# Performance work log

Hardware: AMD Instinct MI355X
Metric: run time of the kernel (lower is better)

Reference implementation:

```python
import jax, jax.numpy as jnp
import numpy as np

B, C, D = 2, 2048, 1024   # batch, seq_len, hidden_size
I = 2048                  # intermediate_size (GLU hidden)
E, K = 8, 2               # n_experts, top_k
CF = 1.25                 # capacity factor


def setup_inputs() -> dict:
    key = jax.random.key(0)
    k1, k2, k3, k4 = jax.random.split(key, 4)
    scale = 0.02
    return {
        "hidden_states": jax.random.normal(k1, (B, C, D), jnp.float32),
        "Wg": jax.random.normal(k2, (E, D), jnp.float32) * scale,      # router gate weight [E, d]
        "W1": jax.random.normal(k3, (E, D, 2 * I), jnp.float32) * scale,  # expert in-proj
        "W2": jax.random.normal(k4, (E, I, D), jnp.float32) * scale,      # expert out-proj
    }


def reference(hidden_states, Wg, W1, W2):
    Bx, Cx, d = hidden_states.shape
    N = Bx * Cx
    cap = int(N * K * CF / E)  # exp_capacity (static)
    x = hidden_states.reshape(N, d)

    # --- router (eval mode: no noise) ---
    logits = x @ Wg.T                          # [N, E]
    top_v, top_i = jax.lax.top_k(logits, K)    # [N, K]
    gates = jax.nn.softmax(top_v, axis=-1)     # [N, K]

    # --- greedy capacity-limited assignment (token-major, then k), vectorized ---
    flat_e = top_i.reshape(N * K)              # expert id per (token, k) slot, in loop order
    gates_f = gates.reshape(N * K)
    tok = jnp.repeat(jnp.arange(N), K)         # token id per slot
    onehot = jax.nn.one_hot(flat_e, E, dtype=jnp.int32)
    pos = jnp.cumsum(onehot, axis=0) - 1       # running count per expert
    pos_f = jnp.take_along_axis(pos, flat_e[:, None], axis=1)[:, 0]
    keep = pos_f < cap                         # slots beyond capacity are dropped
    pos_safe = jnp.where(keep, pos_f, cap)     # out-of-range -> dropped by mode='drop'

    # --- dispatch: exp_batches[e, pos] = x[token] ---
    exp_batches = jnp.zeros((E, cap, d), x.dtype).at[flat_e, pos_safe].set(x[tok], mode='drop')

    # --- per-expert GLU MLP (batched over experts) ---
    h = jnp.einsum('ecd,edf->ecf', exp_batches, W1)       # [E, cap, 2I]
    inp, gate = jnp.split(h, 2, axis=-1)
    h = jax.nn.gelu(inp, approximate=False) * gate        # exact gelu, matches torch
    exp_out = jnp.einsum('eci,eid->ecd', h, W2)           # [E, cap, d]

    # --- combine: equals exp_mask.view(N,-1) @ exp_out.view(-1,d) ---
    gathered = exp_out[flat_e, jnp.minimum(pos_safe, cap - 1)]  # [N*K, d]
    contrib = jnp.where(keep, gates_f, 0.0)[:, None] * gathered
    out = jax.ops.segment_sum(contrib, tok, num_segments=N)    # [N, d]
    return out.reshape(Bx, Cx, d)
```

## Files before the change

kernel.cpp:

```cpp
#include <hip/hip_runtime.h>
#include <hip/hip_bf16.h>
#include <math.h>

#define N_TOK 4096
#define DIM   1024
#define NEXP  8
#define IDIM  2048
#define TWOI  4096
#define CAP   1280

using short8  = __attribute__((ext_vector_type(8))) short;
using floatx4 = __attribute__((ext_vector_type(4))) float;

__device__ __forceinline__ unsigned short f2b(float f) {
  __hip_bfloat16 h = __float2bfloat16(f);
  return *reinterpret_cast<unsigned short*>(&h);
}

__device__ __forceinline__ void async16(const unsigned short* g, unsigned short* l) {
  __builtin_amdgcn_global_load_lds(
      (const __attribute__((address_space(1))) unsigned int*)g,
      (__attribute__((address_space(3))) unsigned int*)l,
      16, 0, 0);
}


__global__ __launch_bounds__(256) void conv_x_kernel(const float* __restrict__ x,
                                                     unsigned short* __restrict__ xb) {
  int i = (blockIdx.x * 256 + threadIdx.x) * 4;
  float4 v = *reinterpret_cast<const float4*>(x + i);
  ushort4 o;
  o.x = f2b(v.x); o.y = f2b(v.y); o.z = f2b(v.z); o.w = f2b(v.w);
  *reinterpret_cast<ushort4*>(xb + i) = o;
}

__global__ __launch_bounds__(256) void transpose_kernel(const float* __restrict__ src,
                                                        unsigned short* __restrict__ dst,
                                                        int R, int C) {
  __shared__ float tile[32][33];
  int e  = blockIdx.z;
  int c0 = blockIdx.x * 32, r0 = blockIdx.y * 32;
  int tx = threadIdx.x & 31, ty = threadIdx.x >> 5;
  const float* s = src + (size_t)e * R * C;
  unsigned short* d = dst + (size_t)e * R * C;
#pragma unroll
  for (int i = 0; i < 4; i++) {
    int r = ty + i * 8;
    tile[r][tx] = s[(size_t)(r0 + r) * C + c0 + tx];
  }
  __syncthreads();
#pragma unroll
  for (int i = 0; i < 4; i++) {
    int c = ty + i * 8;
    d[(size_t)(c0 + c) * R + r0 + tx] = f2b(tile[tx][c]);
  }
}

__global__ __launch_bounds__(256) void router_kernel(const float* __restrict__ x,
                                                     const float* __restrict__ Wg,
                                                     int* __restrict__ top_i,
                                                     float* __restrict__ gates) {
  __shared__ float wg[NEXP * DIM];
  int tid = threadIdx.x;
  for (int i = tid * 4; i < NEXP * DIM; i += 256 * 4) {
    *reinterpret_cast<float4*>(wg + i) = *reinterpret_cast<const float4*>(Wg + i);
  }
  __syncthreads();
  int wave = tid >> 6, lane = tid & 63;
  int t = blockIdx.x * 4 + wave;
  const float* xr = x + (size_t)t * DIM;
  double acc[NEXP];
#pragma unroll
  for (int e = 0; e < NEXP; e++) acc[e] = 0.0;
  for (int i = lane; i < DIM; i += 64) {
    double xv = (double)xr[i];
#pragma unroll
    for (int e = 0; e < NEXP; e++) acc[e] += xv * (double)wg[e * DIM + i];
  }
#pragma unroll
  for (int e = 0; e < NEXP; e++) {
#pragma unroll
    for (int m = 1; m < 64; m <<= 1) acc[e] += __shfl_xor(acc[e], m, 64);
  }
  if (lane == 0) {
    int i0 = 0; double v0 = acc[0];
    for (int e = 1; e < NEXP; e++) { if (acc[e] > v0) { v0 = acc[e]; i0 = e; } }
    int i1 = -1; double v1 = -1e300;
    for (int e = 0; e < NEXP; e++) { if (e != i0 && acc[e] > v1) { v1 = acc[e]; i1 = e; } }
    double e1 = exp(v1 - v0);
    float g0 = (float)(1.0 / (1.0 + e1));
    float g1 = (float)(e1 / (1.0 + e1));
    top_i[t * 2] = i0; top_i[t * 2 + 1] = i1;
    gates[t * 2] = g0; gates[t * 2 + 1] = g1;
  }
}

__global__ __launch_bounds__(256) void scan_kernel(const int* __restrict__ top_i,
                                                   const float* __restrict__ gates,
                                                   int* __restrict__ slot_pos,
                                                   float* __restrict__ keepg,
                                                   int* __restrict__ rowtok,
                                                   int* __restrict__ cnt) {
  __shared__ int hist[NEXP][256];
  int t = threadIdx.x;
  int s0 = t * 32;
  int eloc[32];
  int c[NEXP];
#pragma unroll
  for (int e = 0; e < NEXP; e++) c[e] = 0;
#pragma unroll
  for (int j = 0; j < 32; j++) { int e = top_i[s0 + j]; eloc[j] = e; c[e]++; }
#pragma unroll
  for (int e = 0; e < NEXP; e++) hist[e][t] = c[e];
  __syncthreads();
  for (int step = 1; step < 256; step <<= 1) {
    int tmp[NEXP];
#pragma unroll
    for (int e = 0; e < NEXP; e++) tmp[e] = (t >= step) ? hist[e][t - step] : 0;
    __syncthreads();
#pragma unroll
    for (int e = 0; e < NEXP; e++) hist[e][t] += tmp[e];
    __syncthreads();
  }
  int base[NEXP];
#pragma unroll
  for (int e = 0; e < NEXP; e++) base[e] = hist[e][t] - c[e];
  if (t < NEXP) {
    int tot = hist[t][255];
    cnt[t] = tot < CAP ? tot : CAP;
  }
#pragma unroll
  for (int j = 0; j < 32; j++) {
    int s = s0 + j;
    int e = eloc[j];
    int pos = base[e]++;
    bool keep = pos < CAP;
    slot_pos[s] = keep ? pos : 0;
    keepg[s] = keep ? gates[s] : 0.0f;
    if (keep) rowtok[e * CAP + pos] = s >> 1;
  }
}

__global__ __launch_bounds__(256, 3) void gemm1_kernel(const unsigned short* __restrict__ xb,
                                                       const unsigned short* __restrict__ w1t,
                                                       const int* __restrict__ rowtok,
                                                       const int* __restrict__ cnt,
                                                       unsigned short* __restrict__ H) {
  int e  = blockIdx.z;
  int m0 = blockIdx.y * 128;
  int i0 = blockIdx.x * 128;
  int cnte = cnt[e];
  if (m0 >= cnte) return;

  __shared__ __align__(16) unsigned short As[128 * 32];
  __shared__ __align__(16) unsigned short Bi[128 * 32];
  __shared__ __align__(16) unsigned short Bg[128 * 32];

  int tid  = threadIdx.x;
  int lane = tid & 63;
  int wave = tid >> 6;

  int sr0 = wave * 32 + (lane >> 2);
  int sr1 = sr0 + 16;
  int sk  = (lane & 3) * 8;

  int ma0 = m0 + sr0, ma1 = m0 + sr1;
  int tok0 = (ma0 < cnte) ? rowtok[e * CAP + ma0] : 0;
  int tok1 = (ma1 < cnte) ? rowtok[e * CAP + ma1] : 0;

  const unsigned short* w1e = w1t + (size_t)e * TWOI * DIM;
  const unsigned short* gA0  = xb + (size_t)tok0 * DIM + sk;
  const unsigned short* gA1  = xb + (size_t)tok1 * DIM + sk;
  const unsigned short* gBi0 = w1e + (size_t)(i0 + sr0) * DIM + sk;
  const unsigned short* gBi1 = w1e + (size_t)(i0 + sr1) * DIM + sk;
  const unsigned short* gBg0 = w1e + (size_t)(i0 + sr0 + IDIM) * DIM + sk;
  const unsigned short* gBg1 = w1e + (size_t)(i0 + sr1 + IDIM) * DIM + sk;

  unsigned short* lA0  = As + (wave * 2 + 0) * 512;
  unsigned short* lA1  = As + (wave * 2 + 1) * 512;
  unsigned short* lBi0 = Bi + (wave * 2 + 0) * 512;
  unsigned short* lBi1 = Bi + (wave * 2 + 1) * 512;
  unsigned short* lBg0 = Bg + (wave * 2 + 0) * 512;
  unsigned short* lBg1 = Bg + (wave * 2 + 1) * 512;

  int lane16 = lane & 15;
  int quad   = lane >> 4;
  int wm = (wave & 1) * 64;
  int wn = (wave >> 1) * 64;

  floatx4 acc_i[4][4], acc_g[4][4];
#pragma unroll
  for (int i = 0; i < 4; i++)
#pragma unroll
    for (int j = 0; j < 4; j++) {
      acc_i[i][j] = (floatx4){0.f, 0.f, 0.f, 0.f};
      acc_g[i][j] = (floatx4){0.f, 0.f, 0.f, 0.f};
    }

  for (int k0 = 0; k0 < DIM; k0 += 32) {
    __syncthreads();
    async16(gA0 + k0, lA0);
    async16(gA1 + k0, lA1);
    async16(gBi0 + k0, lBi0);
    async16(gBi1 + k0, lBi1);
    async16(gBg0 + k0, lBg0);
    async16(gBg1 + k0, lBg1);
    __syncthreads();

    short8 a[4];
#pragma unroll
    for (int i = 0; i < 4; i++)
      a[i] = *(const short8*)&As[(wm + i * 16 + lane16) * 32 + quad * 8];
#pragma unroll
    for (int j = 0; j < 4; j++) {
      short8 bi = *(const short8*)&Bi[(wn + j * 16 + lane16) * 32 + quad * 8];
#pragma unroll
      for (int i = 0; i < 4; i++)
        acc_i[i][j] = __builtin_amdgcn_mfma_f32_16x16x32_bf16(a[i], bi, acc_i[i][j], 0, 0, 0);
      short8 bg = *(const short8*)&Bg[(wn + j * 16 + lane16) * 32 + quad * 8];
#pragma unroll
      for (int i = 0; i < 4; i++)
        acc_g[i][j] = __builtin_amdgcn_mfma_f32_16x16x32_bf16(a[i], bg, acc_g[i][j], 0, 0, 0);
    }
  }

  unsigned short* He = H + (size_t)e * CAP * IDIM;
#pragma unroll
  for (int i = 0; i < 4; i++) {
#pragma unroll
    for (int r = 0; r < 4; r++) {
      int m = m0 + wm + i * 16 + quad * 4 + r;
#pragma unroll
      for (int j = 0; j < 4; j++) {
        int n = i0 + wn + j * 16 + lane16;
        float vi = acc_i[i][j][r];
        float vg = acc_g[i][j][r];
        float h = 0.5f * vi * (1.0f + erff(vi * 0.70710678118654752f)) * vg;
        He[(size_t)m * IDIM + n] = f2b(h);
      }
    }
  }
}

__global__ __launch_bounds__(256, 3) void gemm2_kernel(const unsigned short* __restrict__ H,
                                                       const unsigned short* __restrict__ w2t,
                                                       const int* __restrict__ cnt,
                                                       float* __restrict__ expout) {
  int e  = blockIdx.z;
  int m0 = blockIdx.y * 128;
  int n0 = blockIdx.x * 128;
  int cnte = cnt[e];
  if (m0 >= cnte) return;

  __shared__ __align__(16) unsigned short As[128 * 32];
  __shared__ __align__(16) unsigned short Bs[128 * 32];

  int tid  = threadIdx.x;
  int lane = tid & 63;
  int wave = tid >> 6;

  int sr0 = wave * 32 + (lane >> 2);
  int sr1 = sr0 + 16;
  int sk  = (lane & 3) * 8;

  const unsigned short* He  = H + (size_t)e * CAP * IDIM;
  const unsigned short* w2e = w2t + (size_t)e * DIM * IDIM;
  const unsigned short* gA0 = He + (size_t)(m0 + sr0) * IDIM + sk;
  const unsigned short* gA1 = He + (size_t)(m0 + sr1) * IDIM + sk;
  const unsigned short* gB0 = w2e + (size_t)(n0 + sr0) * IDIM + sk;
  const unsigned short* gB1 = w2e + (size_t)(n0 + sr1) * IDIM + sk;

  unsigned short* lA0 = As + (wave * 2 + 0) * 512;
  unsigned short* lA1 = As + (wave * 2 + 1) * 512;
  unsigned short* lB0 = Bs + (wave * 2 + 0) * 512;
  unsigned short* lB1 = Bs + (wave * 2 + 1) * 512;

  int lane16 = lane & 15;
  int quad   = lane >> 4;
  int wm = (wave & 1) * 64;
  int wn = (wave >> 1) * 64;

  floatx4 acc[4][4];
#pragma unroll
  for (int i = 0; i < 4; i++)
#pragma unroll
    for (int j = 0; j < 4; j++) acc[i][j] = (floatx4){0.f, 0.f, 0.f, 0.f};

  for (int k0 = 0; k0 < IDIM; k0 += 32) {
    __syncthreads();
    async16(gA0 + k0, lA0);
    async16(gA1 + k0, lA1);
    async16(gB0 + k0, lB0);
    async16(gB1 + k0, lB1);
    __syncthreads();

    short8 a[4];
#pragma unroll
    for (int i = 0; i < 4; i++)
      a[i] = *(const short8*)&As[(wm + i * 16 + lane16) * 32 + quad * 8];
#pragma unroll
    for (int j = 0; j < 4; j++) {
      short8 b = *(const short8*)&Bs[(wn + j * 16 + lane16) * 32 + quad * 8];
#pragma unroll
      for (int i = 0; i < 4; i++)
        acc[i][j] = __builtin_amdgcn_mfma_f32_16x16x32_bf16(a[i], b, acc[i][j], 0, 0, 0);
    }
  }

  float* oute = expout + (size_t)e * CAP * DIM;
#pragma unroll
  for (int i = 0; i < 4; i++) {
#pragma unroll
    for (int r = 0; r < 4; r++) {
      int m = m0 + wm + i * 16 + quad * 4 + r;
#pragma unroll
      for (int j = 0; j < 4; j++) {
        int n = n0 + wn + j * 16 + lane16;
        oute[(size_t)m * DIM + n] = acc[i][j][r];
      }
    }
  }
}

__global__ __launch_bounds__(256) void combine_kernel(const int* __restrict__ top_i,
                                                      const int* __restrict__ slot_pos,
                                                      const float* __restrict__ keepg,
                                                      const float* __restrict__ expout,
                                                      float* __restrict__ out) {
  int t = blockIdx.x;
  int tid = threadIdx.x;
  int e0 = top_i[t * 2], e1 = top_i[t * 2 + 1];
  int p0 = slot_pos[t * 2], p1 = slot_pos[t * 2 + 1];
  float g0 = keepg[t * 2], g1 = keepg[t * 2 + 1];
  const float4* r0 = reinterpret_cast<const float4*>(expout + ((size_t)e0 * CAP + p0) * DIM);
  const float4* r1 = reinterpret_cast<const float4*>(expout + ((size_t)e1 * CAP + p1) * DIM);
  float4 a = r0[tid], b = r1[tid];
  float4 o;
  o.x = g0 * a.x + g1 * b.x;
  o.y = g0 * a.y + g1 * b.y;
  o.z = g0 * a.z + g1 * b.z;
  o.w = g0 * a.w + g1 * b.w;
  reinterpret_cast<float4*>(out + (size_t)t * DIM)[tid] = o;
}

extern "C" void kernel_launch(void* const* d_in, const int* in_sizes, int n_in,
                              void* d_out, int out_size, void* d_ws, size_t ws_size,
                              hipStream_t stream) {
  const float* x  = (const float*)d_in[0];
  const float* Wg = (const float*)d_in[1];
  const float* W1 = (const float*)d_in[2];
  const float* W2 = (const float*)d_in[3];
  float* out = (float*)d_out;

  char* ws = (char*)d_ws;
  size_t off = 0;
  auto alloc = [&](size_t bytes) -> void* {
    void* p = ws + off;
    off = (off + bytes + 255) & ~(size_t)255;
    return p;
  };
  int*   top_i    = (int*)alloc((size_t)N_TOK * 2 * sizeof(int));
  float* gates    = (float*)alloc((size_t)N_TOK * 2 * sizeof(float));
  int*   slot_pos = (int*)alloc((size_t)N_TOK * 2 * sizeof(int));
  float* keepg    = (float*)alloc((size_t)N_TOK * 2 * sizeof(float));
  int*   rowtok   = (int*)alloc((size_t)NEXP * CAP * sizeof(int));
  int*   cnt      = (int*)alloc((size_t)NEXP * sizeof(int));
  unsigned short* xb  = (unsigned short*)alloc((size_t)N_TOK * DIM * 2);
  unsigned short* w1t = (unsigned short*)alloc((size_t)NEXP * TWOI * DIM * 2);
  unsigned short* w2t = (unsigned short*)alloc((size_t)NEXP * DIM * IDIM * 2);
  unsigned short* Hb  = (unsigned short*)alloc((size_t)NEXP * CAP * IDIM * 2);
  float* expout = (float*)alloc((size_t)NEXP * CAP * DIM * sizeof(float));
  if (off > ws_size) return;

  hipLaunchKernelGGL(conv_x_kernel, dim3(N_TOK * DIM / 1024), dim3(256), 0, stream, x, xb);
  hipLaunchKernelGGL(transpose_kernel, dim3(TWOI / 32, DIM / 32, NEXP), dim3(256), 0, stream,
                     W1, w1t, DIM, TWOI);
  hipLaunchKernelGGL(transpose_kernel, dim3(DIM / 32, IDIM / 32, NEXP), dim3(256), 0, stream,
                     W2, w2t, IDIM, DIM);
  hipLaunchKernelGGL(router_kernel, dim3(N_TOK / 4), dim3(256), 0, stream, x, Wg, top_i, gates);
  hipLaunchKernelGGL(scan_kernel, dim3(1), dim3(256), 0, stream,
                     top_i, gates, slot_pos, keepg, rowtok, cnt);
  hipLaunchKernelGGL(gemm1_kernel, dim3(IDIM / 128, CAP / 128, NEXP), dim3(256), 0, stream,
                     xb, w1t, rowtok, cnt, Hb);
  hipLaunchKernelGGL(gemm2_kernel, dim3(DIM / 128, CAP / 128, NEXP), dim3(256), 0, stream,
                     Hb, w2t, cnt, expout);
  hipLaunchKernelGGL(combine_kernel, dim3(N_TOK), dim3(256), 0, stream,
                     top_i, slot_pos, keepg, expout, out);
}
```

Before: 539.7 us.

## Fuse weight transposes, fold x conversion into router, scatter-add combine in gemm2

Merges the two weight transpose launches into one kernel with 64x64 tiles and vectorized loads and stores. Folds the bf16 conversion of x and the zeroing of the output into the router kernel. Widens the scan to 1024 threads and builds per-row token and gate tables. Halves the gemm1 N tile to give more blocks. Removes the expert-output buffer and combine kernel by having gemm2 atomically add gated results straight into the output, which saves a large fp32 write and read-back but adds atomic traffic and makes the summation order nondeterministic.

```diff
diff --git a/kernel.cpp b/kernel.cpp
--- a/kernel.cpp
+++ b/kernel.cpp
@@ -9,6 +9,9 @@
 #define TWOI  4096
 #define CAP   1280
 
+#define W1_BLOCKS (64 * 16 * NEXP)
+#define W2_BLOCKS (16 * 32 * NEXP)
+
 using short8  = __attribute__((ext_vector_type(8))) short;
 using floatx4 = __attribute__((ext_vector_type(4))) float;
 
@@ -24,40 +27,59 @@
       16, 0, 0);
 }
 
-
-__global__ __launch_bounds__(256) void conv_x_kernel(const float* __restrict__ x,
-                                                     unsigned short* __restrict__ xb) {
-  int i = (blockIdx.x * 256 + threadIdx.x) * 4;
-  float4 v = *reinterpret_cast<const float4*>(x + i);
-  ushort4 o;
-  o.x = f2b(v.x); o.y = f2b(v.y); o.z = f2b(v.z); o.w = f2b(v.w);
-  *reinterpret_cast<ushort4*>(xb + i) = o;
-}
-
-__global__ __launch_bounds__(256) void transpose_kernel(const float* __restrict__ src,
-                                                        unsigned short* __restrict__ dst,
-                                                        int R, int C) {
-  __shared__ float tile[32][33];
-  int e  = blockIdx.z;
-  int c0 = blockIdx.x * 32, r0 = blockIdx.y * 32;
-  int tx = threadIdx.x & 31, ty = threadIdx.x >> 5;
-  const float* s = src + (size_t)e * R * C;
-  unsigned short* d = dst + (size_t)e * R * C;
+__global__ __launch_bounds__(256) void trans_kernel(const float* __restrict__ W1,
+                                                    const float* __restrict__ W2,
+                                                    unsigned short* __restrict__ w1t,
+                                                    unsigned short* __restrict__ w2t) {
+  __shared__ float tile[64][65];
+  int bid = blockIdx.x;
+  const float* s; unsigned short* d; int R, C, r0, c0;
+  if (bid < W1_BLOCKS) {
+    int e = bid >> 10;
+    int t = bid & 1023;
+    R = DIM; C = TWOI;
+    r0 = (t & 15) * 64;
+    c0 = (t >> 4) * 64;
+    s = W1 + (size_t)e * R * C;
+    d = w1t + (size_t)e * R * C;
+  } else {
+    int b2 = bid - W1_BLOCKS;
+    int e = b2 >> 9;
+    int t = b2 & 511;
+    R = IDIM; C = DIM;
+    r0 = (t & 31) * 64;
+    c0 = (t >> 5) * 64;
+    s = W2 + (size_t)e * R * C;
+    d = w2t + (size_t)e * R * C;
+  }
+  int tid = threadIdx.x;
+  int tr = tid >> 4, tc = (tid & 15) * 4;
 #pragma unroll
   for (int i = 0; i < 4; i++) {
-    int r = ty + i * 8;
-    tile[r][tx] = s[(size_t)(r0 + r) * C + c0 + tx];
+    float4 v = *reinterpret_cast<const float4*>(&s[(size_t)(r0 + tr + i * 16) * C + c0 + tc]);
+    tile[tr + i * 16][tc]     = v.x;
+    tile[tr + i * 16][tc + 1] = v.y;
+    tile[tr + i * 16][tc + 2] = v.z;
+    tile[tr + i * 16][tc + 3] = v.w;
   }
   __syncthreads();
 #pragma unroll
-  for (int i = 0; i < 4; i++) {
-    int c = ty + i * 8;
-    d[(size_t)(c0 + c) * R + r0 + tx] = f2b(tile[tx][c]);
+  for (int j = 0; j < 4; j++) {
+    int c = (tid >> 4) + j * 16;
+    int r4 = (tid & 15) * 4;
+    ushort4 o;
+    o.x = f2b(tile[r4][c]);
+    o.y = f2b(tile[r4 + 1][c]);
+    o.z = f2b(tile[r4 + 2][c]);
+    o.w = f2b(tile[r4 + 3][c]);
+    *reinterpret_cast<ushort4*>(&d[(size_t)(c0 + c) * R + r0 + r4]) = o;
   }
 }
 
 __global__ __launch_bounds__(256) void router_kernel(const float* __restrict__ x,
                                                      const float* __restrict__ Wg,
+                                                     unsigned short* __restrict__ xb,
+                                                     float* __restrict__ out,
                                                      int* __restrict__ top_i,
                                                      float* __restrict__ gates) {
   __shared__ float wg[NEXP * DIM];
@@ -69,11 +91,16 @@
   int wave = tid >> 6, lane = tid & 63;
   int t = blockIdx.x * 4 + wave;
   const float* xr = x + (size_t)t * DIM;
+  unsigned short* xbr = xb + (size_t)t * DIM;
+  float* outr = out + (size_t)t * DIM;
   double acc[NEXP];
 #pragma unroll
   for (int e = 0; e < NEXP; e++) acc[e] = 0.0;
   for (int i = lane; i < DIM; i += 64) {
-    double xv = (double)xr[i];
+    float xf = xr[i];
+    xbr[i] = f2b(xf);
+    outr[i] = 0.0f;
+    double xv = (double)xf;
 #pragma unroll
     for (int e = 0; e < NEXP; e++) acc[e] += xv * (double)wg[e * DIM + i];
   }
@@ -95,25 +122,24 @@
   }
 }
 
-__global__ __launch_bounds__(256) void scan_kernel(const int* __restrict__ top_i,
-                                                   const float* __restrict__ gates,
-                                                   int* __restrict__ slot_pos,
-                                                   float* __restrict__ keepg,
-                                                   int* __restrict__ rowtok,
-                                                   int* __restrict__ cnt) {
-  __shared__ int hist[NEXP][256];
+__global__ __launch_bounds__(1024) void scan_kernel(const int* __restrict__ top_i,
+                                                    const float* __restrict__ gates,
+                                                    int* __restrict__ rowtok,
+                                                    float* __restrict__ rowgate,
+                                                    int* __restrict__ cnt) {
+  __shared__ int hist[NEXP][1024];
   int t = threadIdx.x;
-  int s0 = t * 32;
-  int eloc[32];
+  int s0 = t * 8;
+  int eloc[8];
   int c[NEXP];
 #pragma unroll
   for (int e = 0; e < NEXP; e++) c[e] = 0;
 #pragma unroll
-  for (int j = 0; j < 32; j++) { int e = top_i[s0 + j]; eloc[j] = e; c[e]++; }
+  for (int j = 0; j < 8; j++) { int e = top_i[s0 + j]; eloc[j] = e; c[e]++; }
 #pragma unroll
   for (int e = 0; e < NEXP; e++) hist[e][t] = c[e];
   __syncthreads();
-  for (int step = 1; step < 256; step <<= 1) {
+  for (int step = 1; step < 1024; step <<= 1) {
     int tmp[NEXP];
 #pragma unroll
     for (int e = 0; e < NEXP; e++) tmp[e] = (t >= step) ? hist[e][t - step] : 0;
@@ -126,18 +152,18 @@
 #pragma unroll
   for (int e = 0; e < NEXP; e++) base[e] = hist[e][t] - c[e];
   if (t < NEXP) {
-    int tot = hist[t][255];
+    int tot = hist[t][1023];
     cnt[t] = tot < CAP ? tot : CAP;
   }
 #pragma unroll
-  for (int j = 0; j < 32; j++) {
+  for (int j = 0; j < 8; j++) {
     int s = s0 + j;
     int e = eloc[j];
     int pos = base[e]++;
-    bool keep = pos < CAP;
-    slot_pos[s] = keep ? pos : 0;
-    keepg[s] = keep ? gates[s] : 0.0f;
-    if (keep) rowtok[e * CAP + pos] = s >> 1;
+    if (pos < CAP) {
+      rowtok[e * CAP + pos] = s >> 1;
+      rowgate[e * CAP + pos] = gates[s];
+    }
   }
 }
 
@@ -148,51 +174,48 @@
                                                        unsigned short* __restrict__ H) {
   int e  = blockIdx.z;
   int m0 = blockIdx.y * 128;
-  int i0 = blockIdx.x * 128;
+  int i0 = blockIdx.x * 64;
   int cnte = cnt[e];
   if (m0 >= cnte) return;
 
   __shared__ __align__(16) unsigned short As[128 * 32];
-  __shared__ __align__(16) unsigned short Bi[128 * 32];
-  __shared__ __align__(16) unsigned short Bg[128 * 32];
+  __shared__ __align__(16) unsigned short Bi[64 * 32];
+  __shared__ __align__(16) unsigned short Bg[64 * 32];
 
   int tid  = threadIdx.x;
   int lane = tid & 63;
   int wave = tid >> 6;
 
-  int sr0 = wave * 32 + (lane >> 2);
-  int sr1 = sr0 + 16;
-  int sk  = (lane & 3) * 8;
-
-  int ma0 = m0 + sr0, ma1 = m0 + sr1;
+  int srA0 = wave * 32 + (lane >> 2);
+  int srA1 = srA0 + 16;
+  int srB  = wave * 16 + (lane >> 2);
+  int sk   = (lane & 3) * 8;
+
+  int ma0 = m0 + srA0, ma1 = m0 + srA1;
   int tok0 = (ma0 < cnte) ? rowtok[e * CAP + ma0] : 0;
   int tok1 = (ma1 < cnte) ? rowtok[e * CAP + ma1] : 0;
 
   const unsigned short* w1e = w1t + (size_t)e * TWOI * DIM;
-  const unsigned short* gA0  = xb + (size_t)tok0 * DIM + sk;
-  const unsigned short* gA1  = xb + (size_t)tok1 * DIM + sk;
-  const unsigned short* gBi0 = w1e + (size_t)(i0 + sr0) * DIM + sk;
-  const unsigned short* gBi1 = w1e + (size_t)(i0 + sr1) * DIM + sk;
-  const unsigned short* gBg0 = w1e + (size_t)(i0 + sr0 + IDIM) * DIM + sk;
-  const unsigned short* gBg1 = w1e + (size_t)(i0 + sr1 + IDIM) * DIM + sk;
-
-  unsigned short* lA0  = As + (wave * 2 + 0) * 512;
-  unsigned short* lA1  = As + (wave * 2 + 1) * 512;
-  unsigned short* lBi0 = Bi + (wave * 2 + 0) * 512;
-  unsigned short* lBi1 = Bi + (wave * 2 + 1) * 512;
-  unsigned short* lBg0 = Bg + (wave * 2 + 0) * 512;
-  unsigned short* lBg1 = Bg + (wave * 2 + 1) * 512;
+  const unsigned short* gA0 = xb + (size_t)tok0 * DIM + sk;
+  const unsigned short* gA1 = xb + (size_t)tok1 * DIM + sk;
+  const unsigned short* gBi = w1e + (size_t)(i0 + srB) * DIM + sk;
+  const unsigned short* gBg = w1e + (size_t)(i0 + srB + IDIM) * DIM + sk;
+
+  unsigned short* lA0 = As + (wave * 2 + 0) * 512;
+  unsigned short* lA1 = As + (wave * 2 + 1) * 512;
+  unsigned short* lBi = Bi + wave * 512;
+  unsigned short* lBg = Bg + wave * 512;
 
   int lane16 = lane & 15;
   int quad   = lane >> 4;
   int wm = (wave & 1) * 64;
-  int wn = (wave >> 1) * 64;
-
-  floatx4 acc_i[4][4], acc_g[4][4];
+  int wn = (wave >> 1) * 32;
+
+  floatx4 acc_i[4][2], acc_g[4][2];
 #pragma unroll
   for (int i = 0; i < 4; i++)
 #pragma unroll
-    for (int j = 0; j < 4; j++) {
+    for (int j = 0; j < 2; j++) {
       acc_i[i][j] = (floatx4){0.f, 0.f, 0.f, 0.f};
       acc_g[i][j] = (floatx4){0.f, 0.f, 0.f, 0.f};
     }
@@ -201,10 +224,8 @@
     __syncthreads();
     async16(gA0 + k0, lA0);
     async16(gA1 + k0, lA1);
-    async16(gBi0 + k0, lBi0);
-    async16(gBi1 + k0, lBi1);
-    async16(gBg0 + k0, lBg0);
-    async16(gBg1 + k0, lBg1);
+    async16(gBi + k0, lBi);
+    async16(gBg + k0, lBg);
     __syncthreads();
 
     short8 a[4];
@@ -212,7 +233,7 @@
     for (int i = 0; i < 4; i++)
       a[i] = *(const short8*)&As[(wm + i * 16 + lane16) * 32 + quad * 8];
 #pragma unroll
-    for (int j = 0; j < 4; j++) {
+    for (int j = 0; j < 2; j++) {
       short8 bi = *(const short8*)&Bi[(wn + j * 16 + lane16) * 32 + quad * 8];
 #pragma unroll
       for (int i = 0; i < 4; i++)
@@ -231,7 +252,7 @@
     for (int r = 0; r < 4; r++) {
       int m = m0 + wm + i * 16 + quad * 4 + r;
 #pragma unroll
-      for (int j = 0; j < 4; j++) {
+      for (int j = 0; j < 2; j++) {
         int n = i0 + wn + j * 16 + lane16;
         float vi = acc_i[i][j][r];
         float vg = acc_g[i][j][r];
@@ -245,7 +266,9 @@
 __global__ __launch_bounds__(256, 3) void gemm2_kernel(const unsigned short* __restrict__ H,
                                                        const unsigned short* __restrict__ w2t,
                                                        const int* __restrict__ cnt,
-                                                       float* __restrict__ expout) {
+                                                       const int* __restrict__ rowtok,
+                                                       const float* __restrict__ rowgate,
+                                                       float* __restrict__ out) {
   int e  = blockIdx.z;
   int m0 = blockIdx.y * 128;
   int n0 = blockIdx.x * 128;
@@ -307,40 +330,23 @@
     }
   }
 
-  float* oute = expout + (size_t)e * CAP * DIM;
 #pragma unroll
   for (int i = 0; i < 4; i++) {
 #pragma unroll
     for (int r = 0; r < 4; r++) {
       int m = m0 + wm + i * 16 + quad * 4 + r;
-#pragma unroll
-      for (int j = 0; j < 4; j++) {
-        int n = n0 + wn + j * 16 + lane16;
-        oute[(size_t)m * DIM + n] = acc[i][j][r];
+      if (m < cnte) {
+        int tok = rowtok[e * CAP + m];
+        float g = rowgate[e * CAP + m];
+        float* orow = out + (size_t)tok * DIM;
+#pragma unroll
+        for (int j = 0; j < 4; j++) {
+          int n = n0 + wn + j * 16 + lane16;
+          atomicAdd(orow + n, g * acc[i][j][r]);
+        }
       }
     }
   }
-}
-
-__global__ __launch_bounds__(256) void combine_kernel(const int* __restrict__ top_i,
-                                                      const int* __restrict__ slot_pos,
-                                                      const float* __restrict__ keepg,
-                                                      const float* __restrict__ expout,
-                                                      float* __restrict__ out) {
-  int t = blockIdx.x;
-  int tid = threadIdx.x;
-  int e0 = top_i[t * 2], e1 = top_i[t * 2 + 1];
-  int p0 = slot_pos[t * 2], p1 = slot_pos[t * 2 + 1];
-  float g0 = keepg[t * 2], g1 = keepg[t * 2 + 1];
-  const float4* r0 = reinterpret_cast<const float4*>(expout + ((size_t)e0 * CAP + p0) * DIM);
-  const float4* r1 = reinterpret_cast<const float4*>(expout + ((size_t)e1 * CAP + p1) * DIM);
-  float4 a = r0[tid], b = r1[tid];
-  float4 o;
-  o.x = g0 * a.x + g1 * b.x;
-  o.y = g0 * a.y + g1 * b.y;
-  o.z = g0 * a.z + g1 * b.z;
-  o.w = g0 * a.w + g1 * b.w;
-  reinterpret_cast<float4*>(out + (size_t)t * DIM)[tid] = o;
 }
 
 extern "C" void kernel_launch(void* const* d_in, const int* in_sizes, int n_in,
@@ -359,31 +365,25 @@
     off = (off + bytes + 255) & ~(size_t)255;
     return p;
   };
-  int*   top_i    = (int*)alloc((size_t)N_TOK * 2 * sizeof(int));
-  float* gates    = (float*)alloc((size_t)N_TOK * 2 * sizeof(float));
-  int*   slot_pos = (int*)alloc((size_t)N_TOK * 2 * sizeof(int));
-  float* keepg    = (float*)alloc((size_t)N_TOK * 2 * sizeof(float));
-  int*   rowtok   = (int*)alloc((size_t)NEXP * CAP * sizeof(int));
-  int*   cnt      = (int*)alloc((size_t)NEXP * sizeof(int));
+  int*   top_i   = (int*)alloc((size_t)N_TOK * 2 * sizeof(int));
+  float* gates   = (float*)alloc((size_t)N_TOK * 2 * sizeof(float));
+  int*   rowtok  = (int*)alloc((size_t)NEXP * CAP * sizeof(int));
+  float* rowgate = (float*)alloc((size_t)NEXP * CAP * sizeof(float));
+  int*   cnt     = (int*)alloc((size_t)NEXP * sizeof(int));
   unsigned short* xb  = (unsigned short*)alloc((size_t)N_TOK * DIM * 2);
   unsigned short* w1t = (unsigned short*)alloc((size_t)NEXP * TWOI * DIM * 2);
   unsigned short* w2t = (unsigned short*)alloc((size_t)NEXP * DIM * IDIM * 2);
   unsigned short* Hb  = (unsigned short*)alloc((size_t)NEXP * CAP * IDIM * 2);
-  float* expout = (float*)alloc((size_t)NEXP * CAP * DIM * sizeof(float));
   if (off > ws_size) return;
 
-  hipLaunchKernelGGL(conv_x_kernel, dim3(N_TOK * DIM / 1024), dim3(256), 0, stream, x, xb);
-  hipLaunchKernelGGL(transpose_kernel, dim3(TWOI / 32, DIM / 32, NEXP), dim3(256), 0, stream,
-                     W1, w1t, DIM, TWOI);
-  hipLaunchKernelGGL(transpose_kernel, dim3(DIM / 32, IDIM / 32, NEXP), dim3(256), 0, stream,
-                     W2, w2t, IDIM, DIM);
-  hipLaunchKernelGGL(router_kernel, dim3(N_TOK / 4), dim3(256), 0, stream, x, Wg, top_i, gates);
-  hipLaunchKernelGGL(scan_kernel, dim3(1), dim3(256), 0, stream,
-                     top_i, gates, slot_pos, keepg, rowtok, cnt);
-  hipLaunchKernelGGL(gemm1_kernel, dim3(IDIM / 128, CAP / 128, NEXP), dim3(256), 0, stream,
+  hipLaunchKernelGGL(trans_kernel, dim3(W1_BLOCKS + W2_BLOCKS), dim3(256), 0, stream,
+                     W1, W2, w1t, w2t);
+  hipLaunchKernelGGL(router_kernel, dim3(N_TOK / 4), dim3(256), 0, stream,
+                     x, Wg, xb, out, top_i, gates);
+  hipLaunchKernelGGL(scan_kernel, dim3(1), dim3(1024), 0, stream,
+                     top_i, gates, rowtok, rowgate, cnt);
+  hipLaunchKernelGGL(gemm1_kernel, dim3(IDIM / 64, CAP / 128, NEXP), dim3(256), 0, stream,
                      xb, w1t, rowtok, cnt, Hb);
   hipLaunchKernelGGL(gemm2_kernel, dim3(DIM / 128, CAP / 128, NEXP), dim3(256), 0, stream,
-                     Hb, w2t, cnt, expout);
-  hipLaunchKernelGGL(combine_kernel, dim3(N_TOK), dim3(256), 0, stream,
-                     top_i, slot_pos, keepg, expout, out);
-}
+                     Hb, w2t, cnt, rowtok, rowgate, out);
+}
```

New measurement: 468.8 us. -13.1%, faster.
